# Kernel optimization log

Hardware: AMD Instinct MI355X
Metric: run time of the kernel (lower is better)

Reference implementation:

```python
import jax, jax.numpy as jnp
import numpy as np
import math

D_MODEL = 1024
N_HEADS = 16
D_HEAD = D_MODEL // N_HEADS
WINDOW = 256
SCALE = 1.0 / math.sqrt(D_HEAD)


def setup_inputs() -> dict:
    key = jax.random.key(0)
    kx, kqkv, kout = jax.random.split(key, 3)
    x = jax.random.normal(kx, (2, 2048, D_MODEL), dtype=jnp.float32)
    # xavier_uniform for nn.Linear weights (shape [out, in] in torch; store as [in, out] for x @ W)
    lim_qkv = math.sqrt(6.0 / (D_MODEL + 3 * D_MODEL))
    W_qkv = jax.random.uniform(kqkv, (D_MODEL, 3 * D_MODEL), dtype=jnp.float32, minval=-lim_qkv, maxval=lim_qkv)
    lim_out = math.sqrt(6.0 / (D_MODEL + D_MODEL))
    W_out = jax.random.uniform(kout, (D_MODEL, D_MODEL), dtype=jnp.float32, minval=-lim_out, maxval=lim_out)
    return {"x": x, "W_qkv": W_qkv, "W_out": W_out}


def _window_mask(seq_len: int) -> jnp.ndarray:
    # causal + sliding window: position i attends to j with i-WINDOW < j <= i
    i = jnp.arange(seq_len)[:, None]
    j = jnp.arange(seq_len)[None, :]
    allowed = (j <= i) & (j > i - WINDOW)
    return jnp.where(allowed, 0.0, -jnp.inf).astype(jnp.float32)


def reference(x, W_qkv, W_out):
    B, S, _ = x.shape
    qkv = x @ W_qkv                                   # [B, S, 3*D]
    qkv = qkv.reshape(B, S, 3, N_HEADS, D_HEAD)
    qkv = jnp.transpose(qkv, (2, 0, 3, 1, 4))         # [3, B, H, S, Dh]
    q, k, v = qkv[0], qkv[1], qkv[2]
    scores = jnp.einsum('bhsd,bhtd->bhst', q, k) * SCALE
    scores = scores + _window_mask(S)[None, None]
    weights = jax.nn.softmax(scores, axis=-1)
    out = jnp.einsum('bhst,bhtd->bhsd', weights, v)   # [B, H, S, Dh]
    out = jnp.transpose(out, (0, 2, 1, 3)).reshape(B, S, D_MODEL)
    return out @ W_out
```

## Files before the change

### kernel.cpp

```cpp
#include <hip/hip_runtime.h>

typedef unsigned short u16;
typedef unsigned int u32;

#define D_MODEL 1024
#define N_HEADS 16
#define D_HEAD 64
#define WIN 256
#define SEQ 2048
#define BATCH 2
#define NROWS (BATCH*SEQ)

typedef short frag_ab __attribute__((ext_vector_type(8)));
typedef float frag_cd __attribute__((ext_vector_type(4)));
typedef u16 u16x8 __attribute__((ext_vector_type(8)));

__device__ __forceinline__ u16 f2bf(float f) {
    union { float f; u32 u; } x; x.f = f;
    u32 r = x.u + 0x7fffu + ((x.u >> 16) & 1u);
    return (u16)(r >> 16);
}
__device__ __forceinline__ float bf2f(u16 v) {
    union { u32 u; float f; } x; x.u = ((u32)v) << 16; return x.f;
}

__device__ __forceinline__ void load_lds16(const void* g, void* l) {
    __builtin_amdgcn_global_load_lds(
        (const __attribute__((address_space(1))) void*)g,
        (__attribute__((address_space(3))) void*)l, 16, 0, 0);
}

__global__ void cast_kernel(const float4* __restrict__ in, ushort4* __restrict__ out, int n4) {
    int idx = blockIdx.x * blockDim.x + threadIdx.x;
    if (idx < n4) {
        float4 v = in[idx];
        ushort4 o;
        o.x = f2bf(v.x); o.y = f2bf(v.y); o.z = f2bf(v.z); o.w = f2bf(v.w);
        out[idx] = o;
    }
}

__global__ void transpose_cast(const float* __restrict__ W, u16* __restrict__ WT, int K, int N,
                               int scale_rows, float scale) {
    __shared__ float tile[32][33];
    int n0 = blockIdx.x * 32, k0 = blockIdx.y * 32;
    int x = threadIdx.x, y = threadIdx.y;
#pragma unroll
    for (int r = 0; r < 4; r++)
        tile[y + 8 * r][x] = W[(size_t)(k0 + y + 8 * r) * N + n0 + x];
    __syncthreads();
#pragma unroll
    for (int r = 0; r < 4; r++) {
        int nrow = n0 + y + 8 * r;
        float v = tile[x][y + 8 * r];
        if (nrow < scale_rows) v *= scale;
        WT[(size_t)nrow * K + k0 + x] = f2bf(v);
    }
}

template <bool BF16_OUT>
__global__ __launch_bounds__(256) void gemm128(const u16* __restrict__ A,
                                               const u16* __restrict__ BT,
                                               void* __restrict__ C,
                                               int M, int N, int K) {
    __shared__ u16 As[128 * 32];
    __shared__ u16 Bs[128 * 32];
    const int tid = threadIdx.x;
    const int m0 = blockIdx.y * 128, n0 = blockIdx.x * 128;
    const int wave = tid >> 6, lane = tid & 63;
    const int wm = (wave >> 1) * 64, wn = (wave & 1) * 64;
    const int lrow = lane & 15, quad = lane >> 4;

    frag_cd acc[4][4] = {};

    const int c0 = tid, c1 = tid + 256;
    const int r0 = c0 >> 2, w0 = c0 & 3;
    const int r1 = c1 >> 2, w1 = c1 & 3;
    const u16* a0 = A + (size_t)(m0 + r0) * K + w0 * 8;
    const u16* a1 = A + (size_t)(m0 + r1) * K + w1 * 8;
    const u16* b0 = BT + (size_t)(n0 + r0) * K + w0 * 8;
    const u16* b1 = BT + (size_t)(n0 + r1) * K + w1 * 8;

    for (int k0 = 0; k0 < K; k0 += 32) {
        __syncthreads();
        load_lds16(a0 + k0, &As[c0 * 8]);
        load_lds16(a1 + k0, &As[c1 * 8]);
        load_lds16(b0 + k0, &Bs[c0 * 8]);
        load_lds16(b1 + k0, &Bs[c1 * 8]);
        __syncthreads();

        frag_ab af[4], bf[4];
#pragma unroll
        for (int t = 0; t < 4; t++) {
            af[t] = *(const frag_ab*)&As[(wm + t * 16 + lrow) * 32 + quad * 8];
            bf[t] = *(const frag_ab*)&Bs[(wn + t * 16 + lrow) * 32 + quad * 8];
        }
#pragma unroll
        for (int mt = 0; mt < 4; mt++)
#pragma unroll
            for (int nt = 0; nt < 4; nt++)
                acc[mt][nt] = __builtin_amdgcn_mfma_f32_16x16x32_bf16(af[mt], bf[nt], acc[mt][nt], 0, 0, 0);
    }

#pragma unroll
    for (int mt = 0; mt < 4; mt++) {
#pragma unroll
        for (int nt = 0; nt < 4; nt++) {
            int col = n0 + wn + nt * 16 + lrow;
#pragma unroll
            for (int r = 0; r < 4; r++) {
                int row = m0 + wm + mt * 16 + quad * 4 + r;
                float v = acc[mt][nt][r];
                if (BF16_OUT) ((u16*)C)[(size_t)row * N + col] = f2bf(v);
                else          ((float*)C)[(size_t)row * N + col] = v;
            }
        }
    }
}

__global__ __launch_bounds__(256) void attn_kernel(const u16* __restrict__ qkv, u16* __restrict__ out) {
    __shared__ u16 Ks[64 * 64];
    __shared__ u16 Vt[64 * 72];
    __shared__ u16 ps[4][16 * 72];

    const int tid = threadIdx.x;
    const int wave = tid >> 6, lane = tid & 63;
    const int quad = lane >> 4, c16 = lane & 15;

    const int qc = blockIdx.x & 31;
    const int h  = (blockIdx.x >> 5) & 15;
    const int b  = blockIdx.x >> 9;
    const int q0 = qc * 64;
    const int qw0 = q0 + wave * 16;

    frag_ab qf[2];
    {
        const u16* qrow = qkv + (size_t)(b * SEQ + qw0 + c16) * 3072 + h * 64;
        qf[0] = *(const frag_ab*)(qrow + quad * 8);
        qf[1] = *(const frag_ab*)(qrow + 32 + quad * 8);
    }

    float m_r[4], l_r[4];
    frag_cd acc[4] = {};
#pragma unroll
    for (int r = 0; r < 4; r++) { m_r[r] = -1e30f; l_r[r] = 0.f; }

    const int ntiles = qc < 4 ? qc + 1 : 5;

    const int krow = wave * 16 + (lane >> 3);
    const int kchunk = (lane & 7) ^ (lane >> 3);
    const int vj = tid & 63, vdblk = tid >> 6;

    for (int t = 0; t < ntiles; t++) {
        const int j0 = q0 - 64 * t;
        __syncthreads();
        {
            const u16* g = qkv + (size_t)(b * SEQ + j0 + krow) * 3072 + 1024 + h * 64 + kchunk * 8;
            load_lds16(g,            &Ks[krow * 64 + (lane & 7) * 8]);
            load_lds16(g + 8 * 3072, &Ks[(krow + 8) * 64 + (lane & 7) * 8]);
        }
        {
            const u16* g = qkv + (size_t)(b * SEQ + j0 + vj) * 3072 + 2048 + h * 64 + vdblk * 16;
            u16x8 v0 = *(const u16x8*)g;
            u16x8 v1 = *(const u16x8*)(g + 8);
#pragma unroll
            for (int dd = 0; dd < 8; dd++) Vt[(vdblk * 16 + dd) * 72 + vj] = v0[dd];
#pragma unroll
            for (int dd = 0; dd < 8; dd++) Vt[(vdblk * 16 + 8 + dd) * 72 + vj] = v1[dd];
        }
        __syncthreads();

        frag_cd s[4] = {};
#pragma unroll
        for (int kb = 0; kb < 4; kb++) {
            frag_ab kf0 = *(const frag_ab*)&Ks[(kb * 16 + c16) * 64 + ((quad    ) ^ (c16 & 7)) * 8];
            frag_ab kf1 = *(const frag_ab*)&Ks[(kb * 16 + c16) * 64 + ((4 + quad) ^ (c16 & 7)) * 8];
            s[kb] = __builtin_amdgcn_mfma_f32_16x16x32_bf16(qf[0], kf0, s[kb], 0, 0, 0);
            s[kb] = __builtin_amdgcn_mfma_f32_16x16x32_bf16(qf[1], kf1, s[kb], 0, 0, 0);
        }

        float mt[4];
#pragma unroll
        for (int reg = 0; reg < 4; reg++) {
            const int i = qw0 + quad * 4 + reg;
#pragma unroll
            for (int kb = 0; kb < 4; kb++) {
                const int j = j0 + kb * 16 + c16;
                if (j > i || j + WIN <= i) s[kb][reg] = -1e30f;
            }
            mt[reg] = fmaxf(fmaxf(s[0][reg], s[1][reg]), fmaxf(s[2][reg], s[3][reg]));
        }
#pragma unroll
        for (int off = 1; off < 16; off <<= 1)
#pragma unroll
            for (int reg = 0; reg < 4; reg++) mt[reg] = fmaxf(mt[reg], __shfl_xor(mt[reg], off));

        float alpha[4], rs[4];
#pragma unroll
        for (int reg = 0; reg < 4; reg++) {
            float mn = fmaxf(m_r[reg], mt[reg]);
            alpha[reg] = __builtin_amdgcn_exp2f(m_r[reg] - mn);
            m_r[reg] = mn;
            rs[reg] = 0.f;
        }
#pragma unroll
        for (int kb = 0; kb < 4; kb++)
#pragma unroll
            for (int reg = 0; reg < 4; reg++) {
                float p = __builtin_amdgcn_exp2f(s[kb][reg] - m_r[reg]);
                u16 pb = f2bf(p);
                ps[wave][(quad * 4 + reg) * 72 + kb * 16 + c16] = pb;
                rs[reg] += bf2f(pb);
            }
#pragma unroll
        for (int off = 1; off < 16; off <<= 1)
#pragma unroll
            for (int reg = 0; reg < 4; reg++) rs[reg] += __shfl_xor(rs[reg], off);
#pragma unroll
        for (int reg = 0; reg < 4; reg++) l_r[reg] = l_r[reg] * alpha[reg] + rs[reg];
#pragma unroll
        for (int dblk = 0; dblk < 4; dblk++)
#pragma unroll
            for (int reg = 0; reg < 4; reg++) acc[dblk][reg] *= alpha[reg];

#pragma unroll
        for (int js = 0; js < 2; js++) {
            frag_ab pf = *(const frag_ab*)&ps[wave][c16 * 72 + js * 32 + quad * 8];
#pragma unroll
            for (int dblk = 0; dblk < 4; dblk++) {
                frag_ab vf = *(const frag_ab*)&Vt[(dblk * 16 + c16) * 72 + js * 32 + quad * 8];
                acc[dblk] = __builtin_amdgcn_mfma_f32_16x16x32_bf16(pf, vf, acc[dblk], 0, 0, 0);
            }
        }
    }

    float inv[4];
#pragma unroll
    for (int reg = 0; reg < 4; reg++) inv[reg] = 1.f / l_r[reg];
#pragma unroll
    for (int dblk = 0; dblk < 4; dblk++)
#pragma unroll
        for (int reg = 0; reg < 4; reg++)
            out[(size_t)(b * SEQ + qw0 + quad * 4 + reg) * 1024 + h * 64 + dblk * 16 + c16] =
                f2bf(acc[dblk][reg] * inv[reg]);
}

extern "C" void kernel_launch(void* const* d_in, const int* in_sizes, int n_in,
                              void* d_out, int out_size, void* d_ws, size_t ws_size,
                              hipStream_t stream) {
    const float* x     = (const float*)d_in[0];
    const float* W_qkv = (const float*)d_in[1];
    const float* W_out = (const float*)d_in[2];
    float* out = (float*)d_out;

    char* ws = (char*)d_ws;
    u16* xb    = (u16*)(ws);
    u16* wqkvT = (u16*)(ws + 8388608);
    u16* woutT = (u16*)(ws + 14680064);
    u16* qkvb  = (u16*)(ws + 16777216);
    u16* attnb = (u16*)(ws + 41943040);

    const float QSCALE = 0.125f * 1.4426950408889634f;

    {
        int n4 = NROWS * D_MODEL / 4;
        cast_kernel<<<(n4 + 255) / 256, 256, 0, stream>>>((const float4*)x, (ushort4*)xb, n4);
        transpose_cast<<<dim3(3 * D_MODEL / 32, D_MODEL / 32), dim3(32, 8), 0, stream>>>(
            W_qkv, wqkvT, D_MODEL, 3 * D_MODEL, D_MODEL, QSCALE);
        transpose_cast<<<dim3(D_MODEL / 32, D_MODEL / 32), dim3(32, 8), 0, stream>>>(
            W_out, woutT, D_MODEL, D_MODEL, 0, 1.0f);
    }
    gemm128<true><<<dim3(3 * D_MODEL / 128, NROWS / 128), 256, 0, stream>>>(xb, wqkvT, qkvb, NROWS, 3 * D_MODEL, D_MODEL);
    attn_kernel<<<BATCH * N_HEADS * (SEQ / 64), 256, 0, stream>>>(qkvb, attnb);
    gemm128<false><<<dim3(D_MODEL / 128, NROWS / 128), 256, 0, stream>>>(attnb, woutT, out, NROWS, D_MODEL, D_MODEL);
}
```

Measured before the change: 174.3 us.

## Use BK=64 swizzled GEMM tiles, smaller out-proj tiles, packed V transpose

The GEMM now loads 64-wide K slices per iteration, with an XOR swizzle on the LDS chunk index to avoid bank conflicts. This halves the number of barrier pairs per K loop. The output projection is templated to 64-row M tiles, doubling its block count to improve occupancy and wave count on the small N=1024 problem. In attention, the V transpose into LDS now writes packed pairs of adjacent key rows as 32-bit stores instead of 16-bit scattered stores. The trade-off is more LDS per block in the GEMM.

New measurement: 158.2 us. 9.2% less time.

```diff
diff --git a/kernel.cpp b/kernel.cpp
--- a/kernel.cpp
+++ b/kernel.cpp
@@ -58,52 +58,58 @@
     }
 }
 
-template <bool BF16_OUT>
-__global__ __launch_bounds__(256) void gemm128(const u16* __restrict__ A,
-                                               const u16* __restrict__ BT,
-                                               void* __restrict__ C,
-                                               int M, int N, int K) {
-    __shared__ u16 As[128 * 32];
-    __shared__ u16 Bs[128 * 32];
+template <bool BF16_OUT, int BM>
+__global__ __launch_bounds__(256) void gemm_bk64(const u16* __restrict__ A,
+                                                 const u16* __restrict__ BT,
+                                                 void* __restrict__ C,
+                                                 int M, int N, int K) {
+    constexpr int MWAVE = BM / 2;
+    constexpr int MT = BM / 32;
+    __shared__ u16 As[BM * 64];
+    __shared__ u16 Bs[128 * 64];
     const int tid = threadIdx.x;
-    const int m0 = blockIdx.y * 128, n0 = blockIdx.x * 128;
+    const int m0 = blockIdx.y * BM, n0 = blockIdx.x * 128;
     const int wave = tid >> 6, lane = tid & 63;
-    const int wm = (wave >> 1) * 64, wn = (wave & 1) * 64;
+    const int wm = (wave >> 1) * MWAVE, wn = (wave & 1) * 64;
     const int lrow = lane & 15, quad = lane >> 4;
 
-    frag_cd acc[4][4] = {};
-
-    const int c0 = tid, c1 = tid + 256;
-    const int r0 = c0 >> 2, w0 = c0 & 3;
-    const int r1 = c1 >> 2, w1 = c1 & 3;
-    const u16* a0 = A + (size_t)(m0 + r0) * K + w0 * 8;
-    const u16* a1 = A + (size_t)(m0 + r1) * K + w1 * 8;
-    const u16* b0 = BT + (size_t)(n0 + r0) * K + w0 * 8;
-    const u16* b1 = BT + (size_t)(n0 + r1) * K + w1 * 8;
-
-    for (int k0 = 0; k0 < K; k0 += 32) {
-        __syncthreads();
-        load_lds16(a0 + k0, &As[c0 * 8]);
-        load_lds16(a1 + k0, &As[c1 * 8]);
-        load_lds16(b0 + k0, &Bs[c0 * 8]);
-        load_lds16(b1 + k0, &Bs[c1 * 8]);
-        __syncthreads();
-
-        frag_ab af[4], bf[4];
-#pragma unroll
-        for (int t = 0; t < 4; t++) {
-            af[t] = *(const frag_ab*)&As[(wm + t * 16 + lrow) * 32 + quad * 8];
-            bf[t] = *(const frag_ab*)&Bs[(wn + t * 16 + lrow) * 32 + quad * 8];
-        }
-#pragma unroll
-        for (int mt = 0; mt < 4; mt++)
-#pragma unroll
-            for (int nt = 0; nt < 4; nt++)
-                acc[mt][nt] = __builtin_amdgcn_mfma_f32_16x16x32_bf16(af[mt], bf[nt], acc[mt][nt], 0, 0, 0);
-    }
-
-#pragma unroll
-    for (int mt = 0; mt < 4; mt++) {
+    frag_cd acc[MT][4] = {};
+
+    const int r0 = tid >> 3;
+    const int w  = (tid & 7) ^ (r0 & 7);
+    const u16* aP = A  + (size_t)(m0 + r0) * K + w * 8;
+    const u16* bP = BT + (size_t)(n0 + r0) * K + w * 8;
+
+    for (int k0 = 0; k0 < K; k0 += 64) {
+        __syncthreads();
+#pragma unroll
+        for (int u = 0; u < BM / 32; u++)
+            load_lds16(aP + (size_t)(32 * u) * K + k0, &As[(tid + 256 * u) * 8]);
+#pragma unroll
+        for (int u = 0; u < 4; u++)
+            load_lds16(bP + (size_t)(32 * u) * K + k0, &Bs[(tid + 256 * u) * 8]);
+        __syncthreads();
+
+#pragma unroll
+        for (int ko = 0; ko < 2; ko++) {
+            const int csel = ((ko * 4 + quad) ^ (lrow & 7)) * 8;
+            frag_ab af[MT], bf[4];
+#pragma unroll
+            for (int t = 0; t < MT; t++)
+                af[t] = *(const frag_ab*)&As[(wm + t * 16 + lrow) * 64 + csel];
+#pragma unroll
+            for (int t = 0; t < 4; t++)
+                bf[t] = *(const frag_ab*)&Bs[(wn + t * 16 + lrow) * 64 + csel];
+#pragma unroll
+            for (int mt = 0; mt < MT; mt++)
+#pragma unroll
+                for (int nt = 0; nt < 4; nt++)
+                    acc[mt][nt] = __builtin_amdgcn_mfma_f32_16x16x32_bf16(af[mt], bf[nt], acc[mt][nt], 0, 0, 0);
+        }
+    }
+
+#pragma unroll
+    for (int mt = 0; mt < MT; mt++) {
 #pragma unroll
         for (int nt = 0; nt < 4; nt++) {
             int col = n0 + wn + nt * 16 + lrow;
@@ -149,7 +155,7 @@
 
     const int krow = wave * 16 + (lane >> 3);
     const int kchunk = (lane & 7) ^ (lane >> 3);
-    const int vj = tid & 63, vdblk = tid >> 6;
+    const int vj2 = (tid & 31) * 2, vd8 = tid >> 5;
 
     for (int t = 0; t < ntiles; t++) {
         const int j0 = q0 - 64 * t;
@@ -160,13 +166,12 @@
             load_lds16(g + 8 * 3072, &Ks[(krow + 8) * 64 + (lane & 7) * 8]);
         }
         {
-            const u16* g = qkv + (size_t)(b * SEQ + j0 + vj) * 3072 + 2048 + h * 64 + vdblk * 16;
-            u16x8 v0 = *(const u16x8*)g;
-            u16x8 v1 = *(const u16x8*)(g + 8);
-#pragma unroll
-            for (int dd = 0; dd < 8; dd++) Vt[(vdblk * 16 + dd) * 72 + vj] = v0[dd];
-#pragma unroll
-            for (int dd = 0; dd < 8; dd++) Vt[(vdblk * 16 + 8 + dd) * 72 + vj] = v1[dd];
+            const u16* g = qkv + (size_t)(b * SEQ + j0 + vj2) * 3072 + 2048 + h * 64 + vd8 * 8;
+            u16x8 va = *(const u16x8*)g;
+            u16x8 vb = *(const u16x8*)(g + 3072);
+#pragma unroll
+            for (int dd = 0; dd < 8; dd++)
+                *(u32*)&Vt[(vd8 * 8 + dd) * 72 + vj2] = (u32)va[dd] | ((u32)vb[dd] << 16);
         }
         __syncthreads();
 
@@ -179,7 +184,7 @@
             s[kb] = __builtin_amdgcn_mfma_f32_16x16x32_bf16(qf[1], kf1, s[kb], 0, 0, 0);
         }
 
-        float mt[4];
+        float mt_[4];
 #pragma unroll
         for (int reg = 0; reg < 4; reg++) {
             const int i = qw0 + quad * 4 + reg;
@@ -188,17 +193,17 @@
                 const int j = j0 + kb * 16 + c16;
                 if (j > i || j + WIN <= i) s[kb][reg] = -1e30f;
             }
-            mt[reg] = fmaxf(fmaxf(s[0][reg], s[1][reg]), fmaxf(s[2][reg], s[3][reg]));
+            mt_[reg] = fmaxf(fmaxf(s[0][reg], s[1][reg]), fmaxf(s[2][reg], s[3][reg]));
         }
 #pragma unroll
         for (int off = 1; off < 16; off <<= 1)
 #pragma unroll
-            for (int reg = 0; reg < 4; reg++) mt[reg] = fmaxf(mt[reg], __shfl_xor(mt[reg], off));
+            for (int reg = 0; reg < 4; reg++) mt_[reg] = fmaxf(mt_[reg], __shfl_xor(mt_[reg], off));
 
         float alpha[4], rs[4];
 #pragma unroll
         for (int reg = 0; reg < 4; reg++) {
-            float mn = fmaxf(m_r[reg], mt[reg]);
+            float mn = fmaxf(m_r[reg], mt_[reg]);
             alpha[reg] = __builtin_amdgcn_exp2f(m_r[reg] - mn);
             m_r[reg] = mn;
             rs[reg] = 0.f;
@@ -270,7 +275,9 @@
         transpose_cast<<<dim3(D_MODEL / 32, D_MODEL / 32), dim3(32, 8), 0, stream>>>(
             W_out, woutT, D_MODEL, D_MODEL, 0, 1.0f);
     }
-    gemm128<true><<<dim3(3 * D_MODEL / 128, NROWS / 128), 256, 0, stream>>>(xb, wqkvT, qkvb, NROWS, 3 * D_MODEL, D_MODEL);
+    gemm_bk64<true, 128><<<dim3(3 * D_MODEL / 128, NROWS / 128), 256, 0, stream>>>(
+        xb, wqkvT, qkvb, NROWS, 3 * D_MODEL, D_MODEL);
     attn_kernel<<<BATCH * N_HEADS * (SEQ / 64), 256, 0, stream>>>(qkvb, attnb);
-    gemm128<false><<<dim3(D_MODEL / 128, NROWS / 128), 256, 0, stream>>>(attnb, woutT, out, NROWS, D_MODEL, D_MODEL);
-}
+    gemm_bk64<false, 64><<<dim3(D_MODEL / 128, NROWS / 64), 256, 0, stream>>>(
+        attnb, woutT, out, NROWS, D_MODEL, D_MODEL);
+}
```
